# Performance work log

Hardware: AMD Instinct MI355X
Metric: run time of the kernel (lower is better)

## Reference

```python
import jax, jax.numpy as jnp
import numpy as np

D_MODEL = 1024
N_HEADS = 16
D_HEAD = D_MODEL // N_HEADS          # 64
FRACTION_TO_ROTATE = 0.25
ROT_DIM = int(FRACTION_TO_ROTATE * D_HEAD)  # 16 (even)
ROPE_BASE = 10000.0


def setup_inputs() -> dict:
    key = jax.random.key(0)
    ks = jax.random.split(key, 10)
    B, S = 2, 2048
    init = lambda k, fan_in, shape: jax.random.normal(k, shape, jnp.float32) / np.sqrt(fan_in)
    return {
        "x": jax.random.normal(ks[0], (B, S, D_MODEL), jnp.float32),
        "Wq": init(ks[1], D_MODEL, (D_MODEL, D_MODEL)),
        "bq": jnp.zeros((D_MODEL,), jnp.float32),
        "Wk": init(ks[2], D_MODEL, (D_MODEL, D_MODEL)),
        "bk": jnp.zeros((D_MODEL,), jnp.float32),
        "Wv": init(ks[3], D_MODEL, (D_MODEL, D_MODEL)),
        "bv": jnp.zeros((D_MODEL,), jnp.float32),
        "Wo": init(ks[4], D_MODEL, (D_MODEL, D_MODEL)),
        "bo": jnp.zeros((D_MODEL,), jnp.float32),
    }


def _apply_partial_rope(t, cos, sin):
    # t: [B, H, S, d_head]; rotate first ROT_DIM dims, pass the rest through.
    rot, rest = t[..., :ROT_DIM], t[..., ROT_DIM:]
    half = ROT_DIM // 2
    t1, t2 = rot[..., :half], rot[..., half:]
    # cos/sin: [S, half] -> broadcast over [B, H]
    r1 = t1 * cos - t2 * sin
    r2 = t1 * sin + t2 * cos
    return jnp.concatenate([r1, r2, rest], axis=-1)


def reference(x, Wq, bq, Wk, bk, Wv, bv, Wo, bo):
    B, S, D = x.shape
    q = (x @ Wq + bq).reshape(B, S, N_HEADS, D_HEAD).transpose(0, 2, 1, 3)
    k = (x @ Wk + bk).reshape(B, S, N_HEADS, D_HEAD).transpose(0, 2, 1, 3)
    v = (x @ Wv + bv).reshape(B, S, N_HEADS, D_HEAD).transpose(0, 2, 1, 3)

    half = ROT_DIM // 2
    inv_freq = 1.0 / (ROPE_BASE ** (jnp.arange(half, dtype=jnp.float32) / half))
    angles = jnp.arange(S, dtype=jnp.float32)[:, None] * inv_freq  # [S, half]
    cos, sin = jnp.cos(angles), jnp.sin(angles)

    q = _apply_partial_rope(q, cos, sin)
    k = _apply_partial_rope(k, cos, sin)

    scale = 1.0 / np.sqrt(D_HEAD).astype(np.float32)
    scores = jnp.einsum("bhqd,bhkd->bhqk", q, k) * scale  # [B,H,S,S]
    causal = jnp.tril(jnp.ones((S, S), dtype=bool))
    scores = jnp.where(causal, scores, jnp.finfo(scores.dtype).min)
    probs = jax.nn.softmax(scores, axis=-1)

    out = jnp.einsum("bhqk,bhkd->bhqd", probs, v)  # [B,H,S,d_head]
    out = out.transpose(0, 2, 1, 3).reshape(B, S, D)
    return out @ Wo + bo
```

## Files before the change

### kernel.cpp

```cpp
#include <hip/hip_runtime.h>
#include <hip/hip_bf16.h>
#include <math.h>

constexpr int DM = 1024;
constexpr int SEQ = 2048;
constexpr int BATCH = 2;
constexpr int NH = 16;
constexpr int DH = 64;
constexpr int MROWS = BATCH * SEQ;
constexpr float SCALE = 0.125f;

typedef __attribute__((ext_vector_type(8))) short short8;
typedef __attribute__((ext_vector_type(4))) float f32x4;
typedef unsigned short ushort_t;

__device__ __forceinline__ unsigned short f2b(float f) {
    __hip_bfloat16 h = __float2bfloat16(f);
    return __builtin_bit_cast(unsigned short, h);
}
__device__ __forceinline__ float b2f(unsigned short u) {
    unsigned int t = ((unsigned int)u) << 16;
    return __builtin_bit_cast(float, t);
}
__device__ __forceinline__ unsigned int cvtpk_bf16(float lo, float hi) {
    unsigned int r;
    asm("v_cvt_pk_bf16_f32 %0, %1, %2" : "=v"(r) : "v"(lo), "v"(hi));
    return r;
}
__device__ __forceinline__ f32x4 mfma16_bf16(uint2 a, uint2 b, f32x4 c) {
    asm("v_mfma_f32_16x16x16_bf16 %0, %1, %2, %0"
        : "+v"(c) : "v"(a), "v"(b));
    return c;
}

__device__ __forceinline__ void gload16(const ushort_t* g, ushort_t* l) {
    __builtin_amdgcn_global_load_lds(
        (const __attribute__((address_space(1))) void*)g,
        (__attribute__((address_space(3))) void*)l, 16, 0, 0);
}

__global__ __launch_bounds__(256) void conv_all(
    const float* __restrict__ x, ushort_t* __restrict__ xb,
    const float* __restrict__ Wq, const float* __restrict__ Wk,
    const float* __restrict__ Wv, const float* __restrict__ Wo,
    ushort_t* __restrict__ Wqt, ushort_t* __restrict__ Wkt,
    ushort_t* __restrict__ Wvt, ushort_t* __restrict__ Wot) {
    const int bid = blockIdx.x;
    if (bid < 2048) {
        const size_t idx = (size_t)bid * 256 + threadIdx.x;
        const float4* src = (const float4*)(x + idx * 8);
        float4 a = src[0], b = src[1];
        short8 v;
        v[0] = (short)f2b(a.x); v[1] = (short)f2b(a.y);
        v[2] = (short)f2b(a.z); v[3] = (short)f2b(a.w);
        v[4] = (short)f2b(b.x); v[5] = (short)f2b(b.y);
        v[6] = (short)f2b(b.z); v[7] = (short)f2b(b.w);
        *(short8*)(xb + idx * 8) = v;
        return;
    }
    const int wid = bid - 2048;
    const int z = wid >> 8;
    const int rem = wid & 255;
    const float* W; ushort_t* Wt;
    switch (z) {
        case 0:  W = Wq; Wt = Wqt; break;
        case 1:  W = Wk; Wt = Wkt; break;
        case 2:  W = Wv; Wt = Wvt; break;
        default: W = Wo; Wt = Wot; break;
    }
    __shared__ float L[64][65];
    const int n0 = (rem & 15) * 64, k0 = (rem >> 4) * 64;
    const int t = threadIdx.x;
    const int tr = t >> 4, tc4 = (t & 15) * 4;
#pragma unroll
    for (int i = 0; i < 4; ++i) {
        int kk = tr + i * 16;
        float4 v = *(const float4*)&W[(size_t)(k0 + kk) * DM + n0 + tc4];
        L[kk][tc4 + 0] = v.x; L[kk][tc4 + 1] = v.y;
        L[kk][tc4 + 2] = v.z; L[kk][tc4 + 3] = v.w;
    }
    __syncthreads();
#pragma unroll
    for (int i = 0; i < 4; ++i) {
        int nn = tr + i * 16;
        ushort4 u;
        u.x = f2b(L[tc4 + 0][nn]); u.y = f2b(L[tc4 + 1][nn]);
        u.z = f2b(L[tc4 + 2][nn]); u.w = f2b(L[tc4 + 3][nn]);
        *(ushort4*)&Wt[(size_t)(n0 + nn) * DM + k0 + tc4] = u;
    }
}

#define BM 128
#define BN 128
#define BKK 32
#define NKT (DM / BKK)

__device__ __forceinline__ void stage_tile(const ushort_t* __restrict__ A,
                                           const ushort_t* __restrict__ B,
                                           int row0, int col0, int kt,
                                           ushort_t* As, ushort_t* Bs, int tid) {
#pragma unroll
    for (int i = 0; i < 2; ++i) {
        int f = i * 256 + tid;
        int sr = f >> 3, p = f & 7;
        int u = p ^ (sr & 7);
        int r = 2 * sr + (u >> 2);
        int c = u & 3;
        gload16(&A[(size_t)(row0 + r) * DM + kt * BKK + c * 8], &As[f * 8]);
        gload16(&B[(size_t)(col0 + r) * DM + kt * BKK + c * 8], &Bs[f * 8]);
    }
}

__device__ __forceinline__ void mfma_core(const ushort_t* __restrict__ A,
                                          const ushort_t* __restrict__ B,
                                          int row0, int col0,
                                          ushort_t* smem, f32x4 (&acc)[4][4]) {
    const int tid = threadIdx.x;
    const int wave = tid >> 6, lane = tid & 63;
    const int lg = lane >> 4, ln = lane & 15;
    const int wr = wave >> 1, wc = wave & 1;

    stage_tile(A, B, row0, col0, 0, smem, smem + 4096, tid);
    __builtin_amdgcn_sched_barrier(0);
    stage_tile(A, B, row0, col0, 1, smem + 8192, smem + 12288, tid);

    for (int kt = 0; kt < NKT; ++kt) {
        if (kt + 1 < NKT)
            asm volatile("s_waitcnt vmcnt(4)" ::: "memory");
        else
            asm volatile("s_waitcnt vmcnt(0)" ::: "memory");
        __builtin_amdgcn_s_barrier();

        if (kt + 2 < NKT) {
            ushort_t* An = smem + ((kt + 2) % 3) * 8192;
            stage_tile(A, B, row0, col0, kt + 2, An, An + 4096, tid);
        }

        const ushort_t* As = smem + (kt % 3) * 8192;
        const ushort_t* Bs = As + 4096;
        short8 af[4], bf[4];
#pragma unroll
        for (int mi = 0; mi < 4; ++mi) {
            int r = wr * 64 + mi * 16 + ln;
            int sr = r >> 1;
            int p = (((r & 1) << 2) | lg) ^ (sr & 7);
            af[mi] = *(const short8*)&As[sr * 64 + p * 8];
        }
#pragma unroll
        for (int ni = 0; ni < 4; ++ni) {
            int r = wc * 64 + ni * 16 + ln;
            int sr = r >> 1;
            int p = (((r & 1) << 2) | lg) ^ (sr & 7);
            bf[ni] = *(const short8*)&Bs[sr * 64 + p * 8];
        }
        __builtin_amdgcn_s_setprio(1);
#pragma unroll
        for (int mi = 0; mi < 4; ++mi)
#pragma unroll
            for (int ni = 0; ni < 4; ++ni)
                acc[mi][ni] = __builtin_amdgcn_mfma_f32_16x16x32_bf16(
                    af[mi], bf[ni], acc[mi][ni], 0, 0, 0);
        __builtin_amdgcn_s_setprio(0);
    }
}

__global__ __launch_bounds__(256) void mfma_gemm_qkv(
    const ushort_t* __restrict__ xb,
    const ushort_t* __restrict__ Wqt, const ushort_t* __restrict__ Wkt,
    const ushort_t* __restrict__ Wvt,
    const float* __restrict__ bq, const float* __restrict__ bk,
    const float* __restrict__ bv,
    ushort_t* __restrict__ qb, ushort_t* __restrict__ kb,
    ushort_t* __restrict__ vtb) {
    const ushort_t* W; const float* bias;
    if (blockIdx.z == 0)      { W = Wqt; bias = bq; }
    else if (blockIdx.z == 1) { W = Wkt; bias = bk; }
    else                      { W = Wvt; bias = bv; }

    const int row0 = blockIdx.y * BM;
    const int col0 = blockIdx.x * BN;
    __shared__ ushort_t smem[24576];
    f32x4 acc[4][4] = {};
    mfma_core(xb, W, row0, col0, smem, acc);

    const int tid = threadIdx.x;
    const int wave = tid >> 6, lane = tid & 63;
    const int lg = lane >> 4, ln = lane & 15;
    const int wr = wave >> 1, wc = wave & 1;
    const bool isV = (blockIdx.z == 2);

    __syncthreads();
    ushort_t* Cs = smem;
#pragma unroll
    for (int mi = 0; mi < 4; ++mi)
#pragma unroll
        for (int ni = 0; ni < 4; ++ni)
#pragma unroll
            for (int r = 0; r < 4; ++r) {
                int mrel = wr * 64 + mi * 16 + lg * 4 + r;
                int nrel = wc * 64 + ni * 16 + ln;
                float v = acc[mi][ni][r] + bias[col0 + nrel];
                Cs[isV ? (nrel * 128 + mrel) : (mrel * 128 + nrel)] = f2b(v);
            }
    __syncthreads();

    if (!isV) {
        ushort_t* out = (blockIdx.z == 0) ? qb : kb;
#pragma unroll
        for (int i = 0; i < 8; ++i) {
            int f = i * 256 + tid;
            int rrow = f >> 4, c8 = f & 15;
            int m = row0 + rrow;
            int b = m >> 11, s = m & (SEQ - 1);
            int n = col0 + c8 * 8;
            int h = n >> 6, d = n & 63;
            short8 val;
            if (d < 16) {
                const ushort_t* base = &Cs[rrow * 128 + (c8 & 8) * 8];
                const bool hi = (d >= 8);
#pragma unroll
                for (int j = 0; j < 8; ++j) {
                    float t1 = b2f(base[j]);
                    float t2 = b2f(base[8 + j]);
                    float invf = __expf(-(float)j * 1.1512925465f);
                    float ang = (float)s * invf;
                    float c_, si_;
                    __sincosf(ang, &si_, &c_);
                    val[j] = (short)f2b(hi ? (t1 * si_ + t2 * c_)
                                           : (t1 * c_ - t2 * si_));
                }
            } else {
                val = *(const short8*)&Cs[rrow * 128 + c8 * 8];
            }
            *(short8*)&out[((size_t)((b * NH + h) * SEQ) + s) * DH + d] = val;
        }
    } else {
#pragma unroll
        for (int i = 0; i < 8; ++i) {
            int f = i * 256 + tid;
            int nrow = f >> 4, c8 = f & 15;
            int n = col0 + nrow;
            int h = n >> 6, d = n & 63;
            int m = row0 + c8 * 8;
            int b = m >> 11, s = m & (SEQ - 1);
            *(short8*)&vtb[((size_t)((b * NH + h) * DH) + d) * SEQ + s] =
                *(const short8*)&Cs[nrow * 128 + c8 * 8];
        }
    }
}

__global__ __launch_bounds__(256) void mfma_gemm_out(
    const ushort_t* __restrict__ ctxb, const ushort_t* __restrict__ Wot,
    const float* __restrict__ bo, float* __restrict__ out) {
    const int row0 = blockIdx.y * BM;
    const int col0 = blockIdx.x * BN;
    __shared__ ushort_t smem[24576];
    f32x4 acc[4][4] = {};
    mfma_core(ctxb, Wot, row0, col0, smem, acc);

    const int tid = threadIdx.x;
    const int wave = tid >> 6, lane = tid & 63;
    const int lg = lane >> 4, ln = lane & 15;
    const int wr = wave >> 1, wc = wave & 1;
#pragma unroll
    for (int mi = 0; mi < 4; ++mi)
#pragma unroll
        for (int ni = 0; ni < 4; ++ni)
#pragma unroll
            for (int r = 0; r < 4; ++r) {
                int m = row0 + wr * 64 + mi * 16 + lg * 4 + r;
                int n = col0 + wc * 64 + ni * 16 + ln;
                out[(size_t)m * DM + n] = acc[mi][ni][r] + bo[n];
            }
}

#define AQT 64
#define AKT 64
#define NQT (SEQ / AQT)

__global__ __launch_bounds__(256) void attn_mfma(
    const ushort_t* __restrict__ qb, const ushort_t* __restrict__ kb,
    const ushort_t* __restrict__ vtb, ushort_t* __restrict__ ctxb,
    ushort_t* __restrict__ opart, float* __restrict__ lpart) {
    constexpr float C1 = 0.18033688f;
    constexpr float M2 = 1.44269504f;
    const int bh = blockIdx.x;
    const int y = blockIdx.y;

    int qt, t0, t1, chunk;
    if (y < 16)      { qt = 16 + y;  t0 = 0;  t1 = 16;     chunk = 0; }
    else if (y < 32) { qt = 47 - y;  t0 = 16; t1 = qt + 1; chunk = 1; }
    else             { qt = 47 - y;  t0 = 0;  t1 = qt + 1; chunk = -1; }
    const int q0 = qt * AQT;

    const int tid = threadIdx.x;
    const int wave = tid >> 6;
    const int lane = tid & 63;
    const int lg = lane >> 4;
    const int ln = lane & 15;

    __shared__ ushort_t KT[2][64 * 64];
    __shared__ ushort_t VT[2][64 * 64];

    const ushort_t* kbase = kb + (size_t)bh * SEQ * DH;
    const ushort_t* vbase = vtb + (size_t)bh * DH * SEQ;
    const int b = bh >> 4, h = bh & 15;

    const ushort_t* qrow = qb + ((size_t)bh * SEQ + q0 + wave * 16 + ln) * DH;
    short8 qf0 = *(const short8*)&qrow[lg * 8];
    short8 qf1 = *(const short8*)&qrow[32 + lg * 8];

    f32x4 o[4];
#pragma unroll
    for (int nt = 0; nt < 4; nt++) o[nt] = f32x4{0.f, 0.f, 0.f, 0.f};
    float l = 0.f;

#pragma unroll
    for (int i = 0; i < 2; i++) {
        int f = i * 256 + tid;
        int r = f >> 3, p = f & 7, c = p ^ (r & 7);
        gload16(&kbase[(size_t)(t0 * AKT + r) * DH + c * 8], &KT[0][f * 8]);
        gload16(&vbase[(size_t)r * SEQ + t0 * AKT + c * 8], &VT[0][f * 8]);
    }

    int cur = 0;
    for (int t = t0; t < t1; ++t) {
        __syncthreads();

        if (t + 1 < t1) {
            const int nb0 = (t + 1) * AKT;
            const int nxt = cur ^ 1;
#pragma unroll
            for (int i = 0; i < 2; i++) {
                int f = i * 256 + tid;
                int r = f >> 3, p = f & 7, c = p ^ (r & 7);
                gload16(&kbase[(size_t)(nb0 + r) * DH + c * 8], &KT[nxt][f * 8]);
                gload16(&vbase[(size_t)r * SEQ + nb0 + c * 8], &VT[nxt][f * 8]);
            }
        }

        float st[4][4];
        __builtin_amdgcn_s_setprio(1);
#pragma unroll
        for (int kt = 0; kt < 4; kt++) {
            f32x4 acc = f32x4{0.f, 0.f, 0.f, 0.f};
            int krow = kt * 16 + ln;
            short8 b0 = *(const short8*)&KT[cur][krow * 64 + ((lg ^ (krow & 7)) * 8)];
            short8 b1 = *(const short8*)&KT[cur][krow * 64 + (((4 + lg) ^ (krow & 7)) * 8)];
            acc = __builtin_amdgcn_mfma_f32_16x16x32_bf16(b0, qf0, acc, 0, 0, 0);
            acc = __builtin_amdgcn_mfma_f32_16x16x32_bf16(b1, qf1, acc, 0, 0, 0);
#pragma unroll
            for (int r = 0; r < 4; r++) st[kt][r] = acc[r];
        }
        __builtin_amdgcn_s_setprio(0);

        if (t == qt) {
            const int qrel = wave * 16 + ln;
#pragma unroll
            for (int kt = 0; kt < 4; kt++)
#pragma unroll
                for (int r = 0; r < 4; r++)
                    if (kt * 16 + lg * 4 + r > qrel) st[kt][r] = -1e30f;
        }

        uint2 pkq[4];
#pragma unroll
        for (int kt = 0; kt < 4; kt++) {
            float pv[4];
#pragma unroll
            for (int r = 0; r < 4; r++) {
                pv[r] = exp2f(fmaf(C1, st[kt][r], -M2));
                l += pv[r];
            }
            pkq[kt].x = cvtpk_bf16(pv[0], pv[1]);
            pkq[kt].y = cvtpk_bf16(pv[2], pv[3]);
        }

        __builtin_amdgcn_s_setprio(1);
#pragma unroll
        for (int nt = 0; nt < 4; nt++) {
            int vrow = nt * 16 + ln;
#pragma unroll
            for (int kt = 0; kt < 4; kt++) {
                int chunk16 = (2 * kt + (lg >> 1)) ^ (vrow & 7);
                uint2 vb = *(const uint2*)&VT[cur][vrow * 64 + chunk16 * 8 + (lg & 1) * 4];
                o[nt] = mfma16_bf16(pkq[kt], vb, o[nt]);
            }
        }
        __builtin_amdgcn_s_setprio(0);

        cur ^= 1;
    }

    l += __shfl_xor(l, 16);
    l += __shfl_xor(l, 32);

    if (chunk >= 0) {
        const int pid = ((bh << 4) + (qt - 16)) * 2 + chunk;
        if (lg == 0) lpart[pid * 64 + wave * 16 + ln] = l;
        ushort_t* ob = opart + (size_t)pid * 4096;
#pragma unroll
        for (int r = 0; r < 4; r++) {
            int qrel = wave * 16 + lg * 4 + r;
#pragma unroll
            for (int nt = 0; nt < 4; nt++)
                ob[qrel * 64 + nt * 16 + ln] = f2b(o[nt][r]);
        }
    } else {
        const float rcp = 1.f / l;
#pragma unroll
        for (int r = 0; r < 4; r++) {
            float invl = __shfl(rcp, (lane & 48) | (lg * 4 + r));
            int qg = q0 + wave * 16 + lg * 4 + r;
            ushort_t* op = ctxb + ((size_t)(b * SEQ + qg)) * DM + h * DH;
#pragma unroll
            for (int nt = 0; nt < 4; nt++)
                op[nt * 16 + ln] = f2b(o[nt][r] * invl);
        }
    }
}

__global__ __launch_bounds__(256) void attn_reduce(
    const ushort_t* __restrict__ opart, const float* __restrict__ lpart,
    ushort_t* __restrict__ ctxb) {
    const int bh = blockIdx.x;
    const int qt = 16 + blockIdx.y;
    const int tid = threadIdx.x;
    const int q = tid >> 2;
    const int d0 = (tid & 3) * 16;

    const int pid0 = ((bh << 4) + (qt - 16)) * 2;
    const ushort_t* o0 = opart + (size_t)pid0 * 4096 + q * 64 + d0;
    const ushort_t* o1 = opart + (size_t)(pid0 + 1) * 4096 + q * 64 + d0;
    const float inv = 1.f / (lpart[pid0 * 64 + q] + lpart[(pid0 + 1) * 64 + q]);

    const int b = bh >> 4, h = bh & 15;
    ushort_t* op = ctxb + ((size_t)(b * SEQ + qt * 64 + q)) * DM + h * DH + d0;
#pragma unroll
    for (int half = 0; half < 2; ++half) {
        short8 a = *(const short8*)&o0[half * 8];
        short8 c = *(const short8*)&o1[half * 8];
        short8 r;
#pragma unroll
        for (int j = 0; j < 8; ++j)
            r[j] = (short)f2b((b2f((unsigned short)a[j]) +
                               b2f((unsigned short)c[j])) * inv);
        *(short8*)&op[half * 8] = r;
    }
}

extern "C" void kernel_launch(void* const* d_in, const int* in_sizes, int n_in,
                              void* d_out, int out_size, void* d_ws, size_t ws_size,
                              hipStream_t stream) {
    const float* x  = (const float*)d_in[0];
    const float* Wq = (const float*)d_in[1];
    const float* bq = (const float*)d_in[2];
    const float* Wk = (const float*)d_in[3];
    const float* bk = (const float*)d_in[4];
    const float* Wv = (const float*)d_in[5];
    const float* bv = (const float*)d_in[6];
    const float* Wo = (const float*)d_in[7];
    const float* bo = (const float*)d_in[8];
    float* out = (float*)d_out;

    constexpr size_t TSZ = (size_t)MROWS * DM;
    constexpr size_t WSZ = (size_t)DM * DM;
    ushort_t* xb  = (ushort_t*)d_ws;
    ushort_t* Wqt = xb + TSZ;
    ushort_t* Wkt = Wqt + WSZ;
    ushort_t* Wvt = Wkt + WSZ;
    ushort_t* Wot = Wvt + WSZ;
    ushort_t* qbp = Wot + WSZ;
    ushort_t* kbp = qbp + TSZ;
    ushort_t* vtp = kbp + TSZ;
    ushort_t* ctxb = vtp + TSZ;

    ushort_t* opart = xb;
    float* lpart = (float*)Wqt;

    conv_all<<<3072, 256, 0, stream>>>(x, xb, Wq, Wk, Wv, Wo, Wqt, Wkt, Wvt, Wot);

    mfma_gemm_qkv<<<dim3(DM / BN, MROWS / BM, 3), 256, 0, stream>>>(
        xb, Wqt, Wkt, Wvt, bq, bk, bv, qbp, kbp, vtp);

    attn_mfma<<<dim3(BATCH * NH, 48), 256, 0, stream>>>(
        qbp, kbp, vtp, ctxb, opart, lpart);
    attn_reduce<<<dim3(BATCH * NH, 16), 256, 0, stream>>>(opart, lpart, ctxb);

    mfma_gemm_out<<<dim3(DM / BN, MROWS / BM), 256, 0, stream>>>(ctxb, Wot, bo, out);
}
```

Before: 114.8 us.

## Fuse Q/K/V projections into one GEMM kernel sharing the x tile

```diff
diff --git a/kernel.cpp b/kernel.cpp
--- a/kernel.cpp
+++ b/kernel.cpp
@@ -164,87 +164,154 @@
     }
 }
 
-__global__ __launch_bounds__(256) void mfma_gemm_qkv(
-    const ushort_t* __restrict__ xb,
-    const ushort_t* __restrict__ Wqt, const ushort_t* __restrict__ Wkt,
-    const ushort_t* __restrict__ Wvt,
+__global__ __launch_bounds__(256) void mfma_gemm_qkv_fused(
+    const ushort_t* __restrict__ xb, const ushort_t* __restrict__ Wt3,
     const float* __restrict__ bq, const float* __restrict__ bk,
     const float* __restrict__ bv,
     ushort_t* __restrict__ qb, ushort_t* __restrict__ kb,
     ushort_t* __restrict__ vtb) {
-    const ushort_t* W; const float* bias;
-    if (blockIdx.z == 0)      { W = Wqt; bias = bq; }
-    else if (blockIdx.z == 1) { W = Wkt; bias = bk; }
-    else                      { W = Wvt; bias = bv; }
-
+    constexpr size_t WSZ = (size_t)DM * DM;
     const int row0 = blockIdx.y * BM;
     const int col0 = blockIdx.x * BN;
-    __shared__ ushort_t smem[24576];
-    f32x4 acc[4][4] = {};
-    mfma_core(xb, W, row0, col0, smem, acc);
-
     const int tid = threadIdx.x;
     const int wave = tid >> 6, lane = tid & 63;
     const int lg = lane >> 4, ln = lane & 15;
     const int wr = wave >> 1, wc = wave & 1;
-    const bool isV = (blockIdx.z == 2);
-
-    __syncthreads();
+
+    __shared__ ushort_t smem[3 * 16384];
+
+    f32x4 acc[3][4][4] = {};
+
+    auto stage = [&](int kt, int s) {
+        ushort_t* base = smem + s * 16384;
+#pragma unroll
+        for (int i = 0; i < 2; ++i) {
+            int f = i * 256 + tid;
+            int sr = f >> 3, p = f & 7;
+            int u = p ^ (sr & 7);
+            int r = 2 * sr + (u >> 2);
+            int c = u & 3;
+            gload16(&xb[(size_t)(row0 + r) * DM + kt * BKK + c * 8], &base[f * 8]);
+        }
+#pragma unroll
+        for (int zz = 0; zz < 3; ++zz)
+#pragma unroll
+            for (int i = 0; i < 2; ++i) {
+                int f = i * 256 + tid;
+                int sr = f >> 3, p = f & 7;
+                int u = p ^ (sr & 7);
+                int r = 2 * sr + (u >> 2);
+                int c = u & 3;
+                gload16(&Wt3[zz * WSZ + (size_t)(col0 + r) * DM + kt * BKK + c * 8],
+                        &base[(1 + zz) * 4096 + f * 8]);
+            }
+    };
+
+    stage(0, 0);
+    __builtin_amdgcn_sched_barrier(0);
+    stage(1, 1);
+
+    for (int kt = 0; kt < NKT; ++kt) {
+        if (kt + 1 < NKT)
+            asm volatile("s_waitcnt vmcnt(8)" ::: "memory");
+        else
+            asm volatile("s_waitcnt vmcnt(0)" ::: "memory");
+        __builtin_amdgcn_s_barrier();
+
+        if (kt + 2 < NKT) stage(kt + 2, (kt + 2) % 3);
+
+        const ushort_t* As = smem + (kt % 3) * 16384;
+        short8 af[4];
+#pragma unroll
+        for (int mi = 0; mi < 4; ++mi) {
+            int r = wr * 64 + mi * 16 + ln;
+            int sr = r >> 1;
+            int p = (((r & 1) << 2) | lg) ^ (sr & 7);
+            af[mi] = *(const short8*)&As[sr * 64 + p * 8];
+        }
+#pragma unroll
+        for (int zz = 0; zz < 3; ++zz) {
+            const ushort_t* Bs = As + (1 + zz) * 4096;
+            short8 bf[4];
+#pragma unroll
+            for (int ni = 0; ni < 4; ++ni) {
+                int r = wc * 64 + ni * 16 + ln;
+                int sr = r >> 1;
+                int p = (((r & 1) << 2) | lg) ^ (sr & 7);
+                bf[ni] = *(const short8*)&Bs[sr * 64 + p * 8];
+            }
+            __builtin_amdgcn_s_setprio(1);
+#pragma unroll
+            for (int mi = 0; mi < 4; ++mi)
+#pragma unroll
+                for (int ni = 0; ni < 4; ++ni)
+                    acc[zz][mi][ni] = __builtin_amdgcn_mfma_f32_16x16x32_bf16(
+                        af[mi], bf[ni], acc[zz][mi][ni], 0, 0, 0);
+            __builtin_amdgcn_s_setprio(0);
+        }
+    }
+
     ushort_t* Cs = smem;
 #pragma unroll
-    for (int mi = 0; mi < 4; ++mi)
-#pragma unroll
-        for (int ni = 0; ni < 4; ++ni)
-#pragma unroll
-            for (int r = 0; r < 4; ++r) {
-                int mrel = wr * 64 + mi * 16 + lg * 4 + r;
-                int nrel = wc * 64 + ni * 16 + ln;
-                float v = acc[mi][ni][r] + bias[col0 + nrel];
-                Cs[isV ? (nrel * 128 + mrel) : (mrel * 128 + nrel)] = f2b(v);
-            }
-    __syncthreads();
-
-    if (!isV) {
-        ushort_t* out = (blockIdx.z == 0) ? qb : kb;
-#pragma unroll
-        for (int i = 0; i < 8; ++i) {
-            int f = i * 256 + tid;
-            int rrow = f >> 4, c8 = f & 15;
-            int m = row0 + rrow;
-            int b = m >> 11, s = m & (SEQ - 1);
-            int n = col0 + c8 * 8;
-            int h = n >> 6, d = n & 63;
-            short8 val;
-            if (d < 16) {
-                const ushort_t* base = &Cs[rrow * 128 + (c8 & 8) * 8];
-                const bool hi = (d >= 8);
-#pragma unroll
-                for (int j = 0; j < 8; ++j) {
-                    float t1 = b2f(base[j]);
-                    float t2 = b2f(base[8 + j]);
-                    float invf = __expf(-(float)j * 1.1512925465f);
-                    float ang = (float)s * invf;
-                    float c_, si_;
-                    __sincosf(ang, &si_, &c_);
-                    val[j] = (short)f2b(hi ? (t1 * si_ + t2 * c_)
-                                           : (t1 * c_ - t2 * si_));
+    for (int zz = 0; zz < 3; ++zz) {
+        const float* bias = (zz == 0) ? bq : (zz == 1) ? bk : bv;
+        const bool isV = (zz == 2);
+        __syncthreads();
+#pragma unroll
+        for (int mi = 0; mi < 4; ++mi)
+#pragma unroll
+            for (int ni = 0; ni < 4; ++ni)
+#pragma unroll
+                for (int r = 0; r < 4; ++r) {
+                    int mrel = wr * 64 + mi * 16 + lg * 4 + r;
+                    int nrel = wc * 64 + ni * 16 + ln;
+                    float v = acc[zz][mi][ni][r] + bias[col0 + nrel];
+                    Cs[isV ? (nrel * 128 + mrel) : (mrel * 128 + nrel)] = f2b(v);
                 }
-            } else {
-                val = *(const short8*)&Cs[rrow * 128 + c8 * 8];
-            }
-            *(short8*)&out[((size_t)((b * NH + h) * SEQ) + s) * DH + d] = val;
-        }
-    } else {
-#pragma unroll
-        for (int i = 0; i < 8; ++i) {
-            int f = i * 256 + tid;
-            int nrow = f >> 4, c8 = f & 15;
-            int n = col0 + nrow;
-            int h = n >> 6, d = n & 63;
-            int m = row0 + c8 * 8;
-            int b = m >> 11, s = m & (SEQ - 1);
-            *(short8*)&vtb[((size_t)((b * NH + h) * DH) + d) * SEQ + s] =
-                *(const short8*)&Cs[nrow * 128 + c8 * 8];
+        __syncthreads();
+
+        if (!isV) {
+            ushort_t* out = (zz == 0) ? qb : kb;
+#pragma unroll
+            for (int i = 0; i < 8; ++i) {
+                int f = i * 256 + tid;
+                int rrow = f >> 4, c8 = f & 15;
+                int m = row0 + rrow;
+                int b = m >> 11, s = m & (SEQ - 1);
+                int n = col0 + c8 * 8;
+                int h = n >> 6, d = n & 63;
+                short8 val;
+                if (d < 16) {
+                    const ushort_t* base = &Cs[rrow * 128 + (c8 & 8) * 8];
+                    const bool hi = (d >= 8);
+#pragma unroll
+                    for (int j = 0; j < 8; ++j) {
+                        float t1 = b2f(base[j]);
+                        float t2 = b2f(base[8 + j]);
+                        float invf = __expf(-(float)j * 1.1512925465f);
+                        float ang = (float)s * invf;
+                        float c_, si_;
+                        __sincosf(ang, &si_, &c_);
+                        val[j] = (short)f2b(hi ? (t1 * si_ + t2 * c_)
+                                               : (t1 * c_ - t2 * si_));
+                    }
+                } else {
+                    val = *(const short8*)&Cs[rrow * 128 + c8 * 8];
+                }
+                *(short8*)&out[((size_t)((b * NH + h) * SEQ) + s) * DH + d] = val;
+            }
+        } else {
+#pragma unroll
+            for (int i = 0; i < 8; ++i) {
+                int f = i * 256 + tid;
+                int nrow = f >> 4, c8 = f & 15;
+                int n = col0 + nrow;
+                int h = n >> 6, d = n & 63;
+                int m = row0 + c8 * 8;
+                int b = m >> 11, s = m & (SEQ - 1);
+                *(short8*)&vtb[((size_t)((b * NH + h) * DH) + d) * SEQ + s] =
+                    *(const short8*)&Cs[nrow * 128 + c8 * 8];
+            }
         }
     }
 }
@@ -480,8 +547,8 @@
 
     conv_all<<<3072, 256, 0, stream>>>(x, xb, Wq, Wk, Wv, Wo, Wqt, Wkt, Wvt, Wot);
 
-    mfma_gemm_qkv<<<dim3(DM / BN, MROWS / BM, 3), 256, 0, stream>>>(
-        xb, Wqt, Wkt, Wvt, bq, bk, bv, qbp, kbp, vtp);
+    mfma_gemm_qkv_fused<<<dim3(DM / BN, MROWS / BM), 256, 0, stream>>>(
+        xb, Wqt, bq, bk, bv, qbp, kbp, vtp);
 
     attn_mfma<<<dim3(BATCH * NH, 48), 256, 0, stream>>>(
         qbp, kbp, vtp, ctxb, opart, lpart);
```

Result: slower. 121.0 us (+5.4%).
